# Kernel optimization log

Measured on AMD Instinct MI355X. Metric: run time of the kernel, lower is better.

## Reference

```python
import jax, jax.numpy as jnp
import numpy as np

NEG_SLOPE = 0.01  # F.leaky_relu default
N_NODES = 50000
N_EDGES = 800000
DIMS = [1, 64, 128, 64, 1]


def _lrelu(x):
    return jnp.where(x >= 0, x, NEG_SLOPE * x)


def _gconv(x, src, dst, W, b, n):
    # DGL GraphConv, norm='none': sum-aggregate src features into dst, then linear.
    # (DGL multiplies first when in_feats > out_feats; identical math since sum is linear.)
    if x.shape[1] > W.shape[1]:
        x = x @ W
        return jax.ops.segment_sum(x[src], dst, num_segments=n) + b
    agg = jax.ops.segment_sum(x[src], dst, num_segments=n)  # [n, d_in]
    return agg @ W + b


def setup_inputs() -> dict:
    key = jax.random.key(0)
    ks = jax.random.split(key, 16)
    inp = {
        "in_feat": jax.random.normal(ks[0], (N_NODES, 1), jnp.float32),
        "src": jax.random.randint(ks[1], (N_EDGES,), 0, N_NODES),
        "dst": jax.random.randint(ks[2], (N_EDGES,), 0, N_NODES),
    }
    for i in range(4):
        fi, fo = DIMS[i], DIMS[i + 1]
        scale = (2.0 / (fi + fo)) ** 0.5  # xavier-style
        inp[f"W{i}"] = jax.random.normal(ks[3 + 2 * i], (fi, fo), jnp.float32) * scale
        inp[f"b{i}"] = jax.random.normal(ks[4 + 2 * i], (fo,), jnp.float32) * 0.01
    return inp


def reference(in_feat, src, dst, W0, b0, W1, b1, W2, b2, W3, b3):
    n = in_feat.shape[0]
    h = _lrelu(_gconv(in_feat, src, dst, W0, b0, n))
    h = _lrelu(_gconv(h, src, dst, W1, b1, n))
    h = _lrelu(_gconv(h, src, dst, W2, b2, n))
    h = _lrelu(_gconv(h, src, dst, W3, b3, n))
    return h[1]  # node index 1, shape (1,)
```

## Files before the change

### kernel.cpp

```cpp
#include <hip/hip_runtime.h>

#define N_NODES 50000
#define N_EDGES 800000
#define NE4 (N_EDGES / 4)
#define NMASKW 1568
#define MAXN1 192
#define S2MAX 1024
#define DMAX  4096
#define E1MAX 1024
#define BK    96
#define SB   ((NE4 + 255) / 256)
#define FGRID 256
#define SUBN 8
#define SUBW 64

#define AS(p, v) __hip_atomic_store((p), (v), __ATOMIC_RELAXED, __HIP_MEMORY_SCOPE_AGENT)

__device__ __forceinline__ float lrelu(float v) { return v >= 0.f ? v : 0.01f * v; }
__device__ __forceinline__ bool mtest(const unsigned int* m, int i) {
    return (m[i >> 5] >> (i & 31)) & 1u;
}

__global__ __launch_bounds__(256) void scan1_k(const int4* __restrict__ dst4,
                                               const int* __restrict__ src,
                                               unsigned int* __restrict__ f1m,
                                               int* __restrict__ e1src, int* __restrict__ cntE1,
                                               int* __restrict__ pos1, int* __restrict__ cnt1) {
    int t = blockIdx.x * 256 + threadIdx.x;
    if (t >= NE4) return;
    int4 d4 = dst4[t];
#define E1(dd, off) \
    if (dd == 1) { \
        int ss = src[t * 4 + off]; \
        int q = atomicAdd(cntE1, 1); \
        if (q < E1MAX) AS(&e1src[q], ss); \
        unsigned int bit = 1u << (ss & 31); \
        unsigned int old = atomicOr(&f1m[ss >> 5], bit); \
        if (!(old & bit)) { int q1 = atomicAdd(cnt1, 1); AS(&pos1[ss], q1); } }
    E1(d4.x, 0) E1(d4.y, 1) E1(d4.z, 2) E1(d4.w, 3)
#undef E1
}

__global__ __launch_bounds__(256) void scan2_k(const int4* __restrict__ dst4,
                                               const int* __restrict__ src,
                                               const unsigned int* __restrict__ f1m,
                                               unsigned int* __restrict__ f2m,
                                               const int* __restrict__ pos1,
                                               int* __restrict__ pos2, int* __restrict__ cnt2,
                                               int2* __restrict__ eD, int* __restrict__ cntD) {
    __shared__ unsigned int msk[NMASKW];
    for (int k = threadIdx.x; k < NMASKW; k += 256) msk[k] = f1m[k];
    __syncthreads();
    int t = blockIdx.x * 256 + threadIdx.x;
    if (t >= NE4) return;
    int4 d4 = dst4[t];
#define E2(dd, off) \
    if (mtest(msk, dd)) { \
        int ss = src[t * 4 + off]; \
        unsigned int bit = 1u << (ss & 31); \
        unsigned int old = atomicOr(&f2m[ss >> 5], bit); \
        if (!(old & bit)) { int q2 = atomicAdd(cnt2, 1); if (q2 < S2MAX) AS(&pos2[ss], q2); } \
        int q = atomicAdd(cntD, 1); \
        if (q < DMAX) { \
            unsigned long long ev = (unsigned long long)(unsigned int)ss | \
                ((unsigned long long)(unsigned int)pos1[dd] << 32); \
            AS((unsigned long long*)&eD[q], ev); } }
    E2(d4.x, 0) E2(d4.y, 1) E2(d4.z, 2) E2(d4.w, 3)
#undef E2
}

__global__ __launch_bounds__(256) void scan3_k(const int4* __restrict__ dst4,
                                               const int* __restrict__ src,
                                               const unsigned int* __restrict__ f2m,
                                               unsigned int* __restrict__ f3m,
                                               const int* __restrict__ pos2,
                                               float* __restrict__ agg0,
                                               int* __restrict__ bucket,
                                               int* __restrict__ slotCnt) {
    __shared__ unsigned int msk[NMASKW];
    for (int k = threadIdx.x; k < NMASKW; k += 256) msk[k] = f2m[k];
    __syncthreads();
    int t = blockIdx.x * 256 + threadIdx.x;
    if (t >= NE4) return;
    int4 d4 = dst4[t];
#define E3(dd, off) \
    if (mtest(msk, dd)) { \
        int ss = src[t * 4 + off]; \
        unsigned int bit = 1u << (ss & 31); \
        unsigned int old = atomicOr(&f3m[ss >> 5], bit); \
        if (!(old & bit)) AS(&agg0[ss], 0.f); \
        int sl = pos2[dd]; \
        if ((unsigned)sl < S2MAX) { \
            int bi = atomicAdd(&slotCnt[sl], 1); \
            if (bi < BK) AS(&bucket[sl * BK + bi], ss); } }
    E3(d4.x, 0) E3(d4.y, 1) E3(d4.z, 2) E3(d4.w, 3)
#undef E3
}

__global__ __launch_bounds__(256) void scan4_k(const int4* __restrict__ dst4,
                                               const int4* __restrict__ src4,
                                               const float* __restrict__ x,
                                               const unsigned int* __restrict__ f3m,
                                               float* __restrict__ agg0) {
    __shared__ unsigned int msk[NMASKW];
    for (int k = threadIdx.x; k < NMASKW; k += 256) msk[k] = f3m[k];
    __syncthreads();
    int t = blockIdx.x * 256 + threadIdx.x;
    if (t >= NE4) return;
    int4 d4 = dst4[t];
    bool m0 = mtest(msk, d4.x), m1 = mtest(msk, d4.y);
    bool m2 = mtest(msk, d4.z), m3 = mtest(msk, d4.w);
    if (m0 | m1 | m2 | m3) {
        int4 s4 = src4[t];
        if (m0) atomicAdd(&agg0[d4.x], x[s4.x]);
        if (m1) atomicAdd(&agg0[d4.y], x[s4.y]);
        if (m2) atomicAdd(&agg0[d4.z], x[s4.z]);
        if (m3) atomicAdd(&agg0[d4.w], x[s4.w]);
    }
}

struct P6 {
    const int* bucket; const int* slotCnt; const float* agg0;
    const float* W0; const float* b0; const float* W1; const float* b1;
    const float* W2; const float* b2; const float* W3; const float* b3;
    const int* cnt2; const int* pos1; const int* pos2;
    const int2* eD; const int* cntD; const int* e1src; const int* cntE1;
    const int* cnt1; float* t2c; int* sub; int* top; float* out;
};

__global__ __launch_bounds__(256) void fused6_k(P6 p) {
    __shared__ __align__(16) float smem[MAXN1 * 64 + MAXN1];
    __shared__ int lflag;
    const int tid = threadIdx.x;
    int c2 = *p.cnt2; if (c2 > S2MAX) c2 = S2MAX;

    float* xv   = smem;
    float* part = smem + 128;
    float* rowA = smem + 384;
    float* rowH = smem + 448;

    const int g = tid >> 6, j = tid & 63;
    const float w0 = p.W0[j], bb0 = p.b0[j];

    for (int b = blockIdx.x; b < c2; b += FGRID) {
        int cnt = p.slotCnt[b]; if (cnt > BK) cnt = BK;
        if (tid < cnt) xv[tid] = p.agg0[p.bucket[b * BK + tid]];
        __syncthreads();
        float racc = 0.f;
        for (int m = g; m < cnt; m += 4) racc += lrelu(xv[m] * w0 + bb0);
        part[tid] = racc;
        __syncthreads();
        if (tid < 64)
            rowA[tid] = part[tid] + part[64 + tid] + part[128 + tid] + part[192 + tid];
        __syncthreads();
        if (tid < 128) {
            float h = p.b1[tid];
#pragma unroll
            for (int k = 0; k < 64; ++k) h += rowA[k] * p.W1[k * 128 + tid];
            rowH[tid] = lrelu(h);
        }
        __syncthreads();
        if (tid < 64) {
            float a2 = 0.f;
#pragma unroll
            for (int k = 0; k < 128; ++k) a2 += rowH[k] * p.W2[k * 64 + tid];
            AS(&p.t2c[(size_t)b * 64 + tid], a2);
        }
        __syncthreads();
    }

    __syncthreads();
    if (tid == 0) {
        lflag = 0;
        int s = blockIdx.x & (SUBN - 1);
        int old = __hip_atomic_fetch_add(&p.sub[s * SUBW], 1,
                                         __ATOMIC_RELAXED, __HIP_MEMORY_SCOPE_AGENT);
        if (old == (FGRID / SUBN) - 1) {
            int o2 = __hip_atomic_fetch_add(p.top, 1,
                                            __ATOMIC_RELAXED, __HIP_MEMORY_SCOPE_AGENT);
            lflag = (o2 == SUBN - 1);
        }
    }
    __syncthreads();
    if (!lflag) return;

    {
        float* acc = smem;
        float* t3s = smem + MAXN1 * 64;
        int c1 = *p.cnt1;  if (c1 > MAXN1) c1 = MAXN1;
        int cD = *p.cntD;  if (cD > DMAX) cD = DMAX;
        int cE = *p.cntE1; if (cE > E1MAX) cE = E1MAX;
        for (int k = tid; k < c1 * 64; k += 256) acc[k] = 0.f;
        __syncthreads();
        int widx = tid >> 6;
        for (int idx = widx; idx < cD; idx += 4) {
            int2 e = p.eD[idx];
            int s2 = p.pos2[e.x];
            if (e.y < c1 && (unsigned)s2 < (unsigned)c2)
                atomicAdd(&acc[e.y * 64 + j], p.t2c[(size_t)s2 * 64 + j]);
        }
        __syncthreads();
        for (int slot = widx; slot < c1; slot += 4) {
            float v = lrelu(acc[slot * 64 + j] + p.b2[j]) * p.W3[j];
            for (int off = 32; off > 0; off >>= 1) v += __shfl_down(v, off, 64);
            if (j == 0) t3s[slot] = v;
        }
        __syncthreads();
        if (tid < 64) {
            float ssum = 0.f;
            for (int k = tid; k < cE; k += 64) ssum += t3s[p.pos1[p.e1src[k]]];
            for (int off = 32; off > 0; off >>= 1) ssum += __shfl_down(ssum, off, 64);
            if (tid == 0) p.out[0] = lrelu(ssum + p.b3[0]);
        }
    }
}

extern "C" void kernel_launch(void* const* d_in, const int* in_sizes, int n_in,
                              void* d_out, int out_size, void* d_ws, size_t ws_size,
                              hipStream_t stream) {
    const float* x   = (const float*)d_in[0];
    const int*   src = (const int*)d_in[1];
    const int*   dst = (const int*)d_in[2];
    const float* W0 = (const float*)d_in[3];  const float* b0 = (const float*)d_in[4];
    const float* W1 = (const float*)d_in[5];  const float* b1 = (const float*)d_in[6];
    const float* W2 = (const float*)d_in[7];  const float* b2 = (const float*)d_in[8];
    const float* W3 = (const float*)d_in[9];  const float* b3 = (const float*)d_in[10];
    float* out = (float*)d_out;
    const int4* dst4 = (const int4*)dst;
    const int4* src4 = (const int4*)src;

    char* base = (char*)d_ws;
    size_t off = 0;
    auto take = [&](size_t bytes) { char* q = base + off; off += (bytes + 255) & ~(size_t)255; return q; };
    unsigned int* f1m = (unsigned int*)take(NMASKW * 4);
    unsigned int* f2m = (unsigned int*)take(NMASKW * 4);
    unsigned int* f3m = (unsigned int*)take(NMASKW * 4);
    int* cntE1 = (int*)take(4);
    int* cntD  = (int*)take(4);
    int* cnt1  = (int*)take(4);
    int* cnt2  = (int*)take(4);
    int* slotCnt = (int*)take((size_t)S2MAX * 4);
    int* sub   = (int*)take((size_t)SUBN * SUBW * 4);
    int* top   = (int*)take(4);
    size_t zero_bytes = off;
    float* agg0   = (float*)take((size_t)N_NODES * 4);
    float* t2c    = (float*)take((size_t)S2MAX * 64 * 4);
    int*   e1src  = (int*)take((size_t)E1MAX * 4);
    int2*  eD     = (int2*)take((size_t)DMAX * 8);
    int*   bucket = (int*)take((size_t)S2MAX * BK * 4);
    int*   pos1   = (int*)take((size_t)N_NODES * 4);
    int*   pos2   = (int*)take((size_t)N_NODES * 4);

    hipMemsetAsync(base, 0, zero_bytes, stream);

    scan1_k<<<SB, 256, 0, stream>>>(dst4, src, f1m, e1src, cntE1, pos1, cnt1);
    scan2_k<<<SB, 256, 0, stream>>>(dst4, src, f1m, f2m, pos1, pos2, cnt2, eD, cntD);
    scan3_k<<<SB, 256, 0, stream>>>(dst4, src, f2m, f3m, pos2, agg0, bucket, slotCnt);
    scan4_k<<<SB, 256, 0, stream>>>(dst4, src4, x, f3m, agg0);

    P6 hp;
    hp.bucket = bucket; hp.slotCnt = slotCnt; hp.agg0 = agg0;
    hp.W0 = W0; hp.b0 = b0; hp.W1 = W1; hp.b1 = b1;
    hp.W2 = W2; hp.b2 = b2; hp.W3 = W3; hp.b3 = b3;
    hp.cnt2 = cnt2; hp.pos1 = pos1; hp.pos2 = pos2;
    hp.eD = eD; hp.cntD = cntD; hp.e1src = e1src; hp.cntE1 = cntE1;
    hp.cnt1 = cnt1; hp.t2c = t2c; hp.sub = sub; hp.top = top; hp.out = out;
    fused6_k<<<FGRID, 256, 0, stream>>>(hp);
}
```

Before: 156.0 us.

## Scatter layer-2 rows into global accumulator inside per-slot loop instead of last block

The final serial phase in the last-arriving block used to gather layer-2 results over all D-edges into shared memory. Now each block, after computing a slot's row, scans a pre-remapped edge list (built in scan4 with pos2 lookups baked in) and atomically adds its row into a small global accumulator. This distributes the aggregation across blocks and shortens the serial tail. In exchange, every slot iteration rescans all D-edges and adds global atomics, plus some extra work in scan4.

```diff
diff --git a/kernel.cpp b/kernel.cpp
--- a/kernel.cpp
+++ b/kernel.cpp
@@ -101,11 +101,27 @@
                                                const int4* __restrict__ src4,
                                                const float* __restrict__ x,
                                                const unsigned int* __restrict__ f3m,
-                                               float* __restrict__ agg0) {
+                                               float* __restrict__ agg0,
+                                               const int2* __restrict__ eD,
+                                               const int* __restrict__ cntD,
+                                               const int* __restrict__ pos2,
+                                               int2* __restrict__ eDr) {
     __shared__ unsigned int msk[NMASKW];
+    int g = blockIdx.x * 256 + threadIdx.x;
+    {
+        int cD = *cntD; if (cD > DMAX) cD = DMAX;
+        if (g < cD) {
+            int2 e = eD[g];
+            int sl = pos2[e.x];
+            unsigned long long ev =
+                (unsigned long long)(unsigned int)((unsigned)sl < S2MAX ? sl : -1) |
+                ((unsigned long long)(unsigned int)e.y << 32);
+            AS((unsigned long long*)&eDr[g], ev);
+        }
+    }
     for (int k = threadIdx.x; k < NMASKW; k += 256) msk[k] = f3m[k];
     __syncthreads();
-    int t = blockIdx.x * 256 + threadIdx.x;
+    int t = g;
     if (t >= NE4) return;
     int4 d4 = dst4[t];
     bool m0 = mtest(msk, d4.x), m1 = mtest(msk, d4.y);
@@ -119,27 +135,27 @@
     }
 }
 
-struct P6 {
+struct P7 {
     const int* bucket; const int* slotCnt; const float* agg0;
     const float* W0; const float* b0; const float* W1; const float* b1;
     const float* W2; const float* b2; const float* W3; const float* b3;
-    const int* cnt2; const int* pos1; const int* pos2;
-    const int2* eD; const int* cntD; const int* e1src; const int* cntE1;
-    const int* cnt1; float* t2c; int* sub; int* top; float* out;
+    const int* cnt2; const int* pos1;
+    const int2* eDr; const int* cntD; const int* e1src; const int* cntE1;
+    const int* cnt1; float* gacc; int* sub; int* top; float* out;
 };
 
-__global__ __launch_bounds__(256) void fused6_k(P6 p) {
-    __shared__ __align__(16) float smem[MAXN1 * 64 + MAXN1];
+__global__ __launch_bounds__(256) void fused7_k(P7 p) {
+    __shared__ float xv[128];
+    __shared__ float part[256];
+    __shared__ float rowA[64];
+    __shared__ float rowH[128];
+    __shared__ float rowT[64];
+    __shared__ float t3s[MAXN1];
     __shared__ int lflag;
     const int tid = threadIdx.x;
+    const int g = tid >> 6, j = tid & 63;
     int c2 = *p.cnt2; if (c2 > S2MAX) c2 = S2MAX;
-
-    float* xv   = smem;
-    float* part = smem + 128;
-    float* rowA = smem + 384;
-    float* rowH = smem + 448;
-
-    const int g = tid >> 6, j = tid & 63;
+    int cD = *p.cntD; if (cD > DMAX) cD = DMAX;
     const float w0 = p.W0[j], bb0 = p.b0[j];
 
     for (int b = blockIdx.x; b < c2; b += FGRID) {
@@ -164,7 +180,21 @@
             float a2 = 0.f;
 #pragma unroll
             for (int k = 0; k < 128; ++k) a2 += rowH[k] * p.W2[k * 64 + tid];
-            AS(&p.t2c[(size_t)b * 64 + tid], a2);
+            rowT[tid] = a2;
+        }
+        __syncthreads();
+        for (int base = 0; base < cD; base += 256) {
+            int i = base + tid;
+            int2 e = make_int2(-1, -1);
+            if (i < cD) e = p.eDr[i];
+            bool m = (e.x == b);
+            unsigned long long bal = __ballot(m);
+            while (bal) {
+                int bit = __builtin_ctzll(bal); bal &= bal - 1;
+                int sl1 = __shfl(e.y, bit, 64);
+                if ((unsigned)sl1 < MAXN1)
+                    atomicAdd(&p.gacc[sl1 * 64 + j], rowT[j]);
+            }
         }
         __syncthreads();
     }
@@ -185,23 +215,11 @@
     if (!lflag) return;
 
     {
-        float* acc = smem;
-        float* t3s = smem + MAXN1 * 64;
         int c1 = *p.cnt1;  if (c1 > MAXN1) c1 = MAXN1;
-        int cD = *p.cntD;  if (cD > DMAX) cD = DMAX;
         int cE = *p.cntE1; if (cE > E1MAX) cE = E1MAX;
-        for (int k = tid; k < c1 * 64; k += 256) acc[k] = 0.f;
-        __syncthreads();
         int widx = tid >> 6;
-        for (int idx = widx; idx < cD; idx += 4) {
-            int2 e = p.eD[idx];
-            int s2 = p.pos2[e.x];
-            if (e.y < c1 && (unsigned)s2 < (unsigned)c2)
-                atomicAdd(&acc[e.y * 64 + j], p.t2c[(size_t)s2 * 64 + j]);
-        }
-        __syncthreads();
         for (int slot = widx; slot < c1; slot += 4) {
-            float v = lrelu(acc[slot * 64 + j] + p.b2[j]) * p.W3[j];
+            float v = lrelu(p.gacc[slot * 64 + j] + p.b2[j]) * p.W3[j];
             for (int off = 32; off > 0; off >>= 1) v += __shfl_down(v, off, 64);
             if (j == 0) t3s[slot] = v;
         }
@@ -242,11 +260,12 @@
     int* slotCnt = (int*)take((size_t)S2MAX * 4);
     int* sub   = (int*)take((size_t)SUBN * SUBW * 4);
     int* top   = (int*)take(4);
+    float* gacc = (float*)take((size_t)MAXN1 * 64 * 4);
     size_t zero_bytes = off;
     float* agg0   = (float*)take((size_t)N_NODES * 4);
-    float* t2c    = (float*)take((size_t)S2MAX * 64 * 4);
     int*   e1src  = (int*)take((size_t)E1MAX * 4);
     int2*  eD     = (int2*)take((size_t)DMAX * 8);
+    int2*  eDr    = (int2*)take((size_t)DMAX * 8);
     int*   bucket = (int*)take((size_t)S2MAX * BK * 4);
     int*   pos1   = (int*)take((size_t)N_NODES * 4);
     int*   pos2   = (int*)take((size_t)N_NODES * 4);
@@ -256,14 +275,14 @@
     scan1_k<<<SB, 256, 0, stream>>>(dst4, src, f1m, e1src, cntE1, pos1, cnt1);
     scan2_k<<<SB, 256, 0, stream>>>(dst4, src, f1m, f2m, pos1, pos2, cnt2, eD, cntD);
     scan3_k<<<SB, 256, 0, stream>>>(dst4, src, f2m, f3m, pos2, agg0, bucket, slotCnt);
-    scan4_k<<<SB, 256, 0, stream>>>(dst4, src4, x, f3m, agg0);
-
-    P6 hp;
+    scan4_k<<<SB, 256, 0, stream>>>(dst4, src4, x, f3m, agg0, eD, cntD, pos2, eDr);
+
+    P7 hp;
     hp.bucket = bucket; hp.slotCnt = slotCnt; hp.agg0 = agg0;
     hp.W0 = W0; hp.b0 = b0; hp.W1 = W1; hp.b1 = b1;
     hp.W2 = W2; hp.b2 = b2; hp.W3 = W3; hp.b3 = b3;
-    hp.cnt2 = cnt2; hp.pos1 = pos1; hp.pos2 = pos2;
-    hp.eD = eD; hp.cntD = cntD; hp.e1src = e1src; hp.cntE1 = cntE1;
-    hp.cnt1 = cnt1; hp.t2c = t2c; hp.sub = sub; hp.top = top; hp.out = out;
-    fused6_k<<<FGRID, 256, 0, stream>>>(hp);
-}
+    hp.cnt2 = cnt2; hp.pos1 = pos1;
+    hp.eDr = eDr; hp.cntD = cntD; hp.e1src = e1src; hp.cntE1 = cntE1;
+    hp.cnt1 = cnt1; hp.gacc = gacc; hp.sub = sub; hp.top = top; hp.out = out;
+    fused7_k<<<FGRID, 256, 0, stream>>>(hp);
+}
```

New measurement: 128.8 us. 17.5% less time.
